# Kernel optimization log

Hardware: AMD Instinct MI355X
Metric: run time of the kernel (lower is better)

## Reference

```python
import jax, jax.numpy as jnp
import numpy as np

B, SQ, SK, H, NH = 2, 2048, 2048, 1024, 16
HD = H // NH  # 64


def setup_inputs() -> dict:
    key = jax.random.key(0)
    ks = jax.random.split(key, 12)
    s = 1.0 / np.sqrt(H)
    inp = {
        "query": jax.random.normal(ks[0], (B, SQ, H), jnp.float32),
        "key": jax.random.normal(ks[1], (B, SK, H), jnp.float32),
        "value": jax.random.normal(ks[2], (B, SK, H), jnp.float32),
        # lower-triangular causal mask [B, SQ, SK]; nonzero = attend
        "causal_mask": jnp.broadcast_to(
            jnp.tril(jnp.ones((SQ, SK), jnp.int32)), (B, SQ, SK)
        ),
        "Wq": jax.random.uniform(ks[3], (H, H), jnp.float32, -s, s),
        "bq": jnp.zeros((H,), jnp.float32),
        "Wk": jax.random.uniform(ks[4], (H, H), jnp.float32, -s, s),
        "bk": jnp.zeros((H,), jnp.float32),
        "Wv": jax.random.uniform(ks[5], (H, H), jnp.float32, -s, s),
        "bv": jnp.zeros((H,), jnp.float32),
        "Wo": jax.random.uniform(ks[6], (H, H), jnp.float32, -s, s),
        "bo": jnp.zeros((H,), jnp.float32),
        "ln_g": jnp.ones((H,), jnp.float32),
        "ln_b": jnp.zeros((H,), jnp.float32),
    }
    return inp


def _layer_norm(x, g, b, eps=1e-5):
    mu = jnp.mean(x, axis=-1, keepdims=True)
    var = jnp.var(x, axis=-1, keepdims=True)
    return (x - mu) * jax.lax.rsqrt(var + eps) * g + b


def reference(query, key, value, causal_mask, Wq, bq, Wk, bk, Wv, bv, Wo, bo, ln_g, ln_b):
    # projections (torch Linear: x @ W.T + b)
    q = (query @ Wq.T + bq).reshape(B, SQ, NH, HD)
    k = (key @ Wk.T + bk).reshape(B, SK, NH, HD)
    v = (value @ Wv.T + bv).reshape(B, SK, NH, HD)
    # scores [B, NH, SQ, SK]
    scores = jnp.einsum("bqhd,bkhd->bhqk", q, k) / np.sqrt(HD).astype(np.float32)
    scores = jnp.where(causal_mask[:, None, :, :] == 0, -jnp.inf, scores)
    attn = jax.nn.softmax(scores, axis=-1)
    # dropout is identity in eval mode
    out = jnp.einsum("bhqk,bkhd->bqhd", attn, v).reshape(B, SQ, H)
    out = out @ Wo.T + bo
    return _layer_norm(query + out, ln_g, ln_b)
```

## Files before the change

### kernel.cpp

```cpp
#include <hip/hip_runtime.h>
#include <hip/hip_bf16.h>

#define SQL 2048
#define SKL 2048
#define HH  1024
#define NHH 16
#define HDD 64
#define BB  2
#define MM  (BB*SQL)

typedef __attribute__((ext_vector_type(8))) short short8;
typedef __attribute__((ext_vector_type(4))) short short4v;
typedef __attribute__((ext_vector_type(4))) float f32x4;
typedef unsigned short u16;

__device__ inline u16 f2bf(float f) {
    unsigned int u = __float_as_uint(f);
    u += 0x7fffu + ((u >> 16) & 1u);
    return (u16)(u >> 16);
}

__device__ inline unsigned int bf2_bits(float a, float b) {
    __hip_bfloat162 h = __float22bfloat162_rn(make_float2(a, b));
    unsigned int r;
    __builtin_memcpy(&r, &h, 4);
    return r;
}

__device__ inline void gl_lds16(const void* g, void* l) {
    __builtin_amdgcn_global_load_lds(
        (const __attribute__((address_space(1))) unsigned int*)g,
        (__attribute__((address_space(3))) unsigned int*)l, 16, 0, 0);
}

__global__ __launch_bounds__(256) void cvt_all_kernel(
    const float* __restrict__ q, const float* __restrict__ k, const float* __restrict__ v,
    const float* __restrict__ wq, const float* __restrict__ wk,
    const float* __restrict__ wv, const float* __restrict__ wo,
    u16* __restrict__ xq, u16* __restrict__ xk, u16* __restrict__ xv,
    u16* __restrict__ wqb, u16* __restrict__ wkb, u16* __restrict__ wvb, u16* __restrict__ wob)
{
    int b = blockIdx.x;
    const float* src; u16* dst;
    if      (b < 4096)  { src = q;  dst = xq; }
    else if (b < 8192)  { src = k;  dst = xk;  b -= 4096; }
    else if (b < 12288) { src = v;  dst = xv;  b -= 8192; }
    else if (b < 13312) { src = wq; dst = wqb; b -= 12288; }
    else if (b < 14336) { src = wk; dst = wkb; b -= 13312; }
    else if (b < 15360) { src = wv; dst = wvb; b -= 14336; }
    else                { src = wo; dst = wob; b -= 15360; }
    int i = (b * 256 + threadIdx.x) * 4;
    float4 vv = *(const float4*)(src + i);
    ushort4 oo;
    oo.x = f2bf(vv.x); oo.y = f2bf(vv.y); oo.z = f2bf(vv.z); oo.w = f2bf(vv.w);
    *(ushort4*)(dst + i) = oo;
}

__global__ __launch_bounds__(256) void proj_kernel(
    const u16* __restrict__ xq, const u16* __restrict__ xk, const u16* __restrict__ xv,
    const u16* __restrict__ wqb, const u16* __restrict__ wkb, const u16* __restrict__ wvb,
    const float* __restrict__ bq, const float* __restrict__ bk, const float* __restrict__ bv,
    u16* __restrict__ oq, u16* __restrict__ ok, u16* __restrict__ ov)
{
    const int z = blockIdx.z;
    const u16* A      = (z == 0) ? xq  : (z == 1) ? xk  : xv;
    const u16* W      = (z == 0) ? wqb : (z == 1) ? wkb : wvb;
    const float* bias = (z == 0) ? bq  : (z == 1) ? bk  : bv;
    u16* outb         = (z == 0) ? oq  : (z == 1) ? ok  : ov;
    const float scale = (z == 0) ? 0.125f * 1.4426950408889634f : 1.0f;

    __shared__ u16 pool[2 * 128 * 64];
    u16* lds_a = pool;
    u16* lds_b = pool + 128 * 64;

    const int t = threadIdx.x;
    const int lane = t & 63;
    const int quad = lane >> 4;
    const int lo = lane & 15;
    const int wv = t >> 6;
    const int wm = (wv >> 1) * 64, wn = (wv & 1) * 64;
    const int m0 = blockIdx.x * 128;
    const int n0 = blockIdx.y * 128;

    f32x4 acc[4][4];
#pragma unroll
    for (int i = 0; i < 4; i++)
#pragma unroll
        for (int j = 0; j < 4; j++) acc[i][j] = (f32x4){0.f, 0.f, 0.f, 0.f};

    int rr[4], cc[4];
#pragma unroll
    for (int u = 0; u < 4; u++) {
        int sl = u * 256 + t;
        rr[u] = sl >> 3;
        cc[u] = ((sl & 7) ^ (rr[u] & 7)) * 8;
    }

    for (int k0 = 0; k0 < HH; k0 += 64) {
#pragma unroll
        for (int u = 0; u < 4; u++) {
            gl_lds16(A + (size_t)(m0 + rr[u]) * HH + k0 + cc[u], &lds_a[(u * 256 + t) * 8]);
            gl_lds16(W + (size_t)(n0 + rr[u]) * HH + k0 + cc[u], &lds_b[(u * 256 + t) * 8]);
        }
        __syncthreads();
#pragma unroll
        for (int kk = 0; kk < 2; kk++) {
            short8 af[4], bf[4];
#pragma unroll
            for (int i = 0; i < 4; i++) {
                const int ra = wm + i * 16 + lo;
                const int rb = wn + i * 16 + lo;
                af[i] = *(const short8*)&lds_a[ra * 64 + (((kk * 4 + quad) ^ (ra & 7)) * 8)];
                bf[i] = *(const short8*)&lds_b[rb * 64 + (((kk * 4 + quad) ^ (rb & 7)) * 8)];
            }
            if (z == 2) {
#pragma unroll
                for (int i = 0; i < 4; i++)
#pragma unroll
                    for (int j = 0; j < 4; j++)
                        acc[i][j] = __builtin_amdgcn_mfma_f32_16x16x32_bf16(af[i], bf[j], acc[i][j], 0, 0, 0);
            } else {
#pragma unroll
                for (int i = 0; i < 4; i++)
#pragma unroll
                    for (int j = 0; j < 4; j++)
                        acc[i][j] = __builtin_amdgcn_mfma_f32_16x16x32_bf16(bf[j], af[i], acc[i][j], 0, 0, 0);
            }
        }
        __syncthreads();
    }

    u16* cbuf = &pool[wv * 4096];

    if (z != 2) {
#pragma unroll
        for (int j = 0; j < 4; j++) {
            float4 b4 = *(const float4*)&bias[n0 + wn + j * 16 + quad * 4];
#pragma unroll
            for (int i = 0; i < 4; i++) {
                int tokl = i * 16 + lo;
                int lc = j * 2 + (quad >> 1);
                int phys = lc ^ (tokl & 7);
                uint2 pk;
                pk.x = bf2_bits((acc[i][j][0] + b4.x) * scale, (acc[i][j][1] + b4.y) * scale);
                pk.y = bf2_bits((acc[i][j][2] + b4.z) * scale, (acc[i][j][3] + b4.w) * scale);
                *(uint2*)&cbuf[tokl * 64 + phys * 8 + (quad & 1) * 4] = pk;
            }
        }
        __syncthreads();
#pragma unroll
        for (int it = 0; it < 8; it++) {
            int row = it * 8 + (lane >> 3);
            int lc2 = lane & 7;
            short8 val = *(const short8*)&cbuf[row * 64 + ((lc2 ^ (row & 7)) * 8)];
            int tok = m0 + wm + row;
            int dgb = n0 + wn + lc2 * 8;
            int bi = tok >> 11, s = tok & 2047;
            int head = dgb >> 6, d = dgb & 63;
            *(short8*)&outb[(((size_t)bi * NHH + head) * SQL + s) * HDD + d] = val;
        }
    } else {
#pragma unroll
        for (int j = 0; j < 4; j++) {
            float bsc = bias[n0 + wn + j * 16 + lo];
#pragma unroll
            for (int i = 0; i < 4; i++) {
                int dgl = j * 16 + lo;
                int lc = i * 2 + (quad >> 1);
                int phys = lc ^ (dgl & 7);
                uint2 pk;
                pk.x = bf2_bits(acc[i][j][0] + bsc, acc[i][j][1] + bsc);
                pk.y = bf2_bits(acc[i][j][2] + bsc, acc[i][j][3] + bsc);
                *(uint2*)&cbuf[dgl * 64 + phys * 8 + (quad & 1) * 4] = pk;
            }
        }
        __syncthreads();
#pragma unroll
        for (int it = 0; it < 8; it++) {
            int row = it * 8 + (lane >> 3);
            int lc2 = lane & 7;
            short8 val = *(const short8*)&cbuf[row * 64 + ((lc2 ^ (row & 7)) * 8)];
            int dg = n0 + wn + row;
            int tokb = m0 + wm + lc2 * 8;
            int bi = tokb >> 11, s = tokb & 2047;
            int head = dg >> 6, d = dg & 63;
            *(short8*)&outb[(((size_t)bi * NHH + head) * HDD + d) * SKL + s] = val;
        }
    }
}

__global__ __launch_bounds__(256) void outproj_kernel(
    const u16* __restrict__ A, const u16* __restrict__ W,
    const float* __restrict__ bias, const float* __restrict__ resid,
    float* __restrict__ outf)
{
    __shared__ u16 pool[2 * 128 * 64];
    u16* lds_a = pool;
    u16* lds_b = pool + 128 * 64;

    const int t = threadIdx.x;
    const int lane = t & 63;
    const int quad = lane >> 4;
    const int lo = lane & 15;
    const int wv = t >> 6;
    const int wm = (wv >> 1) * 64, wn = (wv & 1) * 64;
    const int m0 = blockIdx.x * 128;
    const int n0 = blockIdx.y * 128;

    f32x4 acc[4][4];
#pragma unroll
    for (int i = 0; i < 4; i++)
#pragma unroll
        for (int j = 0; j < 4; j++) acc[i][j] = (f32x4){0.f, 0.f, 0.f, 0.f};

    int rr[4], cc[4];
#pragma unroll
    for (int u = 0; u < 4; u++) {
        int sl = u * 256 + t;
        rr[u] = sl >> 3;
        cc[u] = ((sl & 7) ^ (rr[u] & 7)) * 8;
    }

    for (int k0 = 0; k0 < HH; k0 += 64) {
#pragma unroll
        for (int u = 0; u < 4; u++) {
            gl_lds16(A + (size_t)(m0 + rr[u]) * HH + k0 + cc[u], &lds_a[(u * 256 + t) * 8]);
            gl_lds16(W + (size_t)(n0 + rr[u]) * HH + k0 + cc[u], &lds_b[(u * 256 + t) * 8]);
        }
        __syncthreads();
#pragma unroll
        for (int kk = 0; kk < 2; kk++) {
            short8 af[4], bf[4];
#pragma unroll
            for (int i = 0; i < 4; i++) {
                const int ra = wm + i * 16 + lo;
                const int rb = wn + i * 16 + lo;
                af[i] = *(const short8*)&lds_a[ra * 64 + (((kk * 4 + quad) ^ (ra & 7)) * 8)];
                bf[i] = *(const short8*)&lds_b[rb * 64 + (((kk * 4 + quad) ^ (rb & 7)) * 8)];
            }
#pragma unroll
            for (int i = 0; i < 4; i++)
#pragma unroll
                for (int j = 0; j < 4; j++)
                    acc[i][j] = __builtin_amdgcn_mfma_f32_16x16x32_bf16(bf[j], af[i], acc[i][j], 0, 0, 0);
        }
        __syncthreads();
    }

    float* cbuf = (float*)&pool[wv * 4096];

#pragma unroll
    for (int half = 0; half < 2; half++) {
#pragma unroll
        for (int j = 0; j < 4; j++) {
            float4 b4 = *(const float4*)&bias[n0 + wn + j * 16 + quad * 4];
#pragma unroll
            for (int ii = 0; ii < 2; ii++) {
                int i = half * 2 + ii;
                int tl = ii * 16 + lo;
                int lc = j * 4 + quad;
                int phys = lc ^ (tl & 7);
                f32x4 vq;
                vq[0] = acc[i][j][0] + b4.x; vq[1] = acc[i][j][1] + b4.y;
                vq[2] = acc[i][j][2] + b4.z; vq[3] = acc[i][j][3] + b4.w;
                *(f32x4*)&cbuf[tl * 64 + phys * 4] = vq;
            }
        }
        __syncthreads();
#pragma unroll
        for (int it = 0; it < 8; it++) {
            int rowl = it * 4 + (lane >> 4);
            int lc2 = lane & 15;
            f32x4 val = *(const f32x4*)&cbuf[rowl * 64 + ((lc2 ^ (rowl & 7)) * 4)];
            int tok = m0 + wm + half * 32 + rowl;
            int col = n0 + wn + lc2 * 4;
            const float4 rd = *(const float4*)&resid[(size_t)tok * HH + col];
            float4 o;
            o.x = val[0] + rd.x; o.y = val[1] + rd.y;
            o.z = val[2] + rd.z; o.w = val[3] + rd.w;
            *(float4*)&outf[(size_t)tok * HH + col] = o;
        }
        __syncthreads();
    }
}

#define PSTR 72

__global__ __launch_bounds__(256) void attn_kernel(
    const u16* __restrict__ qb, const u16* __restrict__ kb, const u16* __restrict__ vtb,
    u16* __restrict__ attn_out)
{
    __shared__ u16 k_lds[64 * 64];
    __shared__ u16 vt_lds[64 * 64];
    __shared__ u16 p_lds[4 * 16 * PSTR];

    const int t = threadIdx.x;
    const int lane = t & 63;
    const int quad = lane >> 4;
    const int lo = lane & 15;
    const int w = t >> 6;
    const int qt = (SQL / 64 - 1) - (blockIdx.x >> 5);
    const int bh = blockIdx.x & 31;
    const int q0 = qt * 64;

    const u16* qbase = qb + ((size_t)bh * SQL + q0 + w * 16 + lo) * HDD + quad * 8;
    short8 qf0 = *(const short8*)qbase;
    short8 qf1 = *(const short8*)(qbase + 32);

    float m_s = -__builtin_inff(), l_s = 0.f;
    f32x4 o[4];
#pragma unroll
    for (int j = 0; j < 4; j++) o[j] = (f32x4){0.f, 0.f, 0.f, 0.f};

    const int sl0 = t, sl1 = 256 + t;
    const int r0 = sl0 >> 3, c0 = ((sl0 & 7) ^ (r0 & 7)) * 8;
    const int r1 = sl1 >> 3, c1 = ((sl1 & 7) ^ (r1 & 7)) * 8;
    const u16* kbh = kb + (size_t)bh * SKL * HDD;
    const u16* vbh = vtb + (size_t)bh * HDD * SKL;
    u16* ppriv = &p_lds[w * 16 * PSTR];

    for (int kt = 0; kt <= qt; kt++) {
        const int k0 = kt * 64;
        gl_lds16(kbh + (size_t)(k0 + r0) * HDD + c0, &k_lds[sl0 * 8]);
        gl_lds16(kbh + (size_t)(k0 + r1) * HDD + c1, &k_lds[sl1 * 8]);
        gl_lds16(vbh + (size_t)r0 * SKL + k0 + c0, &vt_lds[sl0 * 8]);
        gl_lds16(vbh + (size_t)r1 * SKL + k0 + c1, &vt_lds[sl1 * 8]);
        __syncthreads();

        f32x4 s[4];
#pragma unroll
        for (int nt = 0; nt < 4; nt++) {
            const int row = nt * 16 + lo;
            short8 kf0 = *(const short8*)&k_lds[row * 64 + ((quad ^ (row & 7)) * 8)];
            short8 kf1 = *(const short8*)&k_lds[row * 64 + (((4 + quad) ^ (row & 7)) * 8)];
            s[nt] = (f32x4){0.f, 0.f, 0.f, 0.f};
            s[nt] = __builtin_amdgcn_mfma_f32_16x16x32_bf16(kf0, qf0, s[nt], 0, 0, 0);
            s[nt] = __builtin_amdgcn_mfma_f32_16x16x32_bf16(kf1, qf1, s[nt], 0, 0, 0);
        }
        if (kt == qt) {
            const int ql = w * 16 + lo;
#pragma unroll
            for (int nt = 0; nt < 4; nt++)
#pragma unroll
                for (int r = 0; r < 4; r++)
                    if (nt * 16 + quad * 4 + r > ql) s[nt][r] = -__builtin_inff();
        }

        float mx = s[0][0];
#pragma unroll
        for (int nt = 0; nt < 4; nt++)
#pragma unroll
            for (int r = 0; r < 4; r++) mx = fmaxf(mx, s[nt][r]);
        mx = fmaxf(mx, __shfl_xor(mx, 16));
        mx = fmaxf(mx, __shfl_xor(mx, 32));
        float mnew = fmaxf(m_s, mx);
        float al = __builtin_amdgcn_exp2f(m_s - mnew);
        m_s = mnew;
        float rs = 0.f;
#pragma unroll
        for (int nt = 0; nt < 4; nt++)
#pragma unroll
            for (int r = 0; r < 4; r++) {
                s[nt][r] = __builtin_amdgcn_exp2f(s[nt][r] - m_s);
                rs += s[nt][r];
            }
        rs += __shfl_xor(rs, 16);
        rs += __shfl_xor(rs, 32);
        l_s = l_s * al + rs;

        float alr[4];
#pragma unroll
        for (int r = 0; r < 4; r++) alr[r] = __shfl(al, quad * 4 + r, 16);
#pragma unroll
        for (int nt = 0; nt < 4; nt++)
#pragma unroll
            for (int r = 0; r < 4; r++) o[nt][r] *= alr[r];

#pragma unroll
        for (int nt = 0; nt < 4; nt++) {
            short4v pk;
#pragma unroll
            for (int r = 0; r < 4; r++) pk[r] = (short)f2bf(s[nt][r]);
            *(short4v*)&ppriv[lo * PSTR + nt * 16 + quad * 4] = pk;
        }
        short8 pf0 = *(const short8*)&ppriv[lo * PSTR + quad * 8];
        short8 pf1 = *(const short8*)&ppriv[lo * PSTR + 32 + quad * 8];

#pragma unroll
        for (int nt = 0; nt < 4; nt++) {
            const int row = nt * 16 + lo;
            short8 vf0 = *(const short8*)&vt_lds[row * 64 + ((quad ^ (row & 7)) * 8)];
            short8 vf1 = *(const short8*)&vt_lds[row * 64 + (((4 + quad) ^ (row & 7)) * 8)];
            o[nt] = __builtin_amdgcn_mfma_f32_16x16x32_bf16(pf0, vf0, o[nt], 0, 0, 0);
            o[nt] = __builtin_amdgcn_mfma_f32_16x16x32_bf16(pf1, vf1, o[nt], 0, 0, 0);
        }
        __syncthreads();
    }

    const int b = bh >> 4, h = bh & 15;
    float inv[4];
#pragma unroll
    for (int r = 0; r < 4; r++) inv[r] = 1.0f / __shfl(l_s, quad * 4 + r, 16);
#pragma unroll
    for (int nt = 0; nt < 4; nt++)
#pragma unroll
        for (int r = 0; r < 4; r++) {
            int srow = q0 + w * 16 + quad * 4 + r;
            attn_out[((size_t)b * SQL + srow) * HH + h * HDD + nt * 16 + lo] =
                f2bf(o[nt][r] * inv[r]);
        }
}

__global__ __launch_bounds__(256) void ln_kernel(const float* __restrict__ x,
                                                 const float* __restrict__ g,
                                                 const float* __restrict__ bb,
                                                 float* __restrict__ out)
{
    const int row = blockIdx.x;
    const int t = threadIdx.x;
    const float* xr = x + (size_t)row * HH;
    float4 v = *(const float4*)(xr + t * 4);
    float s1 = v.x + v.y + v.z + v.w;
    float s2 = v.x * v.x + v.y * v.y + v.z * v.z + v.w * v.w;
#pragma unroll
    for (int off = 32; off; off >>= 1) { s1 += __shfl_xor(s1, off); s2 += __shfl_xor(s2, off); }
    __shared__ float red[8];
    if ((t & 63) == 0) { red[(t >> 6) * 2] = s1; red[(t >> 6) * 2 + 1] = s2; }
    __syncthreads();
    s1 = red[0] + red[2] + red[4] + red[6];
    s2 = red[1] + red[3] + red[5] + red[7];
    float mu = s1 * (1.0f / HH);
    float var = s2 * (1.0f / HH) - mu * mu;
    float rstd = rsqrtf(var + 1e-5f);
    float4 gg = *(const float4*)(g + t * 4);
    float4 b4 = *(const float4*)(bb + t * 4);
    float4 o;
    o.x = (v.x - mu) * rstd * gg.x + b4.x;
    o.y = (v.y - mu) * rstd * gg.y + b4.y;
    o.z = (v.z - mu) * rstd * gg.z + b4.z;
    o.w = (v.w - mu) * rstd * gg.w + b4.w;
    *(float4*)(out + (size_t)row * HH + t * 4) = o;
}

extern "C" void kernel_launch(void* const* d_in, const int* in_sizes, int n_in,
                              void* d_out, int out_size, void* d_ws, size_t ws_size,
                              hipStream_t stream)
{
    const float* query = (const float*)d_in[0];
    const float* key   = (const float*)d_in[1];
    const float* value = (const float*)d_in[2];
    const float* Wq = (const float*)d_in[4];
    const float* bq = (const float*)d_in[5];
    const float* Wk = (const float*)d_in[6];
    const float* bk = (const float*)d_in[7];
    const float* Wv = (const float*)d_in[8];
    const float* bv = (const float*)d_in[9];
    const float* Wo = (const float*)d_in[10];
    const float* bo = (const float*)d_in[11];
    const float* ln_g = (const float*)d_in[12];
    const float* ln_b = (const float*)d_in[13];
    float* out = (float*)d_out;

    char* wp = (char*)d_ws;
    auto alloc = [&](size_t bytes) { void* p = (void*)wp; wp += (bytes + 255) & ~(size_t)255; return p; };
    const int nW = HH * HH;
    const int nX = MM * HH;
    u16* wqb = (u16*)alloc((size_t)nW * 2);
    u16* wkb = (u16*)alloc((size_t)nW * 2);
    u16* wvb = (u16*)alloc((size_t)nW * 2);
    u16* wob = (u16*)alloc((size_t)nW * 2);
    u16* xq  = (u16*)alloc((size_t)nX * 2);
    u16* xk  = (u16*)alloc((size_t)nX * 2);
    u16* xv  = (u16*)alloc((size_t)nX * 2);
    u16* qbuf = (u16*)alloc((size_t)nX * 2);
    u16* kbuf = (u16*)alloc((size_t)nX * 2);
    u16* vbuf = (u16*)alloc((size_t)nX * 2);
    u16* attnb = (u16*)alloc((size_t)nX * 2);
    float* projf = (float*)alloc((size_t)nX * 4);

    cvt_all_kernel<<<16384, 256, 0, stream>>>(query, key, value, Wq, Wk, Wv, Wo,
                                              xq, xk, xv, wqb, wkb, wvb, wob);

    proj_kernel<<<dim3(32, 8, 3), 256, 0, stream>>>(
        xq, xk, xv, wqb, wkb, wvb, bq, bk, bv, qbuf, kbuf, vbuf);

    attn_kernel<<<1024, 256, 0, stream>>>(qbuf, kbuf, vbuf, attnb);

    outproj_kernel<<<dim3(32, 8), 256, 0, stream>>>(attnb, wob, bo, query, projf);

    ln_kernel<<<MM, 256, 0, stream>>>(projf, ln_g, ln_b, out);
}
```

Measured before the change: 253.9 us.

## Fuse fp32-to-bf16 activation conversion into projection GEMM and shrink outproj tiles

The separate conversion of query/key/value to bf16 is removed. The projection kernel now loads fp32 activations directly, converts them in registers and stores bf16 into LDS, which drops a full read-write pass over three 16MB inputs. The output projection tile shrinks from 128x128 to 64x128, doubling the grid to 512 blocks for better CU occupancy. In exchange, the projection kernel's A-operand loads are now synchronous register loads instead of async global-to-LDS, which may add latency in the GEMM loop.

```diff
diff --git a/kernel.cpp b/kernel.cpp
--- a/kernel.cpp
+++ b/kernel.cpp
@@ -33,22 +33,17 @@
         (__attribute__((address_space(3))) unsigned int*)l, 16, 0, 0);
 }
 
-__global__ __launch_bounds__(256) void cvt_all_kernel(
-    const float* __restrict__ q, const float* __restrict__ k, const float* __restrict__ v,
+__global__ __launch_bounds__(256) void cvt_w_kernel(
     const float* __restrict__ wq, const float* __restrict__ wk,
     const float* __restrict__ wv, const float* __restrict__ wo,
-    u16* __restrict__ xq, u16* __restrict__ xk, u16* __restrict__ xv,
     u16* __restrict__ wqb, u16* __restrict__ wkb, u16* __restrict__ wvb, u16* __restrict__ wob)
 {
     int b = blockIdx.x;
     const float* src; u16* dst;
-    if      (b < 4096)  { src = q;  dst = xq; }
-    else if (b < 8192)  { src = k;  dst = xk;  b -= 4096; }
-    else if (b < 12288) { src = v;  dst = xv;  b -= 8192; }
-    else if (b < 13312) { src = wq; dst = wqb; b -= 12288; }
-    else if (b < 14336) { src = wk; dst = wkb; b -= 13312; }
-    else if (b < 15360) { src = wv; dst = wvb; b -= 14336; }
-    else                { src = wo; dst = wob; b -= 15360; }
+    if      (b < 1024) { src = wq; dst = wqb; }
+    else if (b < 2048) { src = wk; dst = wkb; b -= 1024; }
+    else if (b < 3072) { src = wv; dst = wvb; b -= 2048; }
+    else               { src = wo; dst = wob; b -= 3072; }
     int i = (b * 256 + threadIdx.x) * 4;
     float4 vv = *(const float4*)(src + i);
     ushort4 oo;
@@ -57,13 +52,13 @@
 }
 
 __global__ __launch_bounds__(256) void proj_kernel(
-    const u16* __restrict__ xq, const u16* __restrict__ xk, const u16* __restrict__ xv,
+    const float* __restrict__ qf, const float* __restrict__ kf, const float* __restrict__ vf,
     const u16* __restrict__ wqb, const u16* __restrict__ wkb, const u16* __restrict__ wvb,
     const float* __restrict__ bq, const float* __restrict__ bk, const float* __restrict__ bv,
     u16* __restrict__ oq, u16* __restrict__ ok, u16* __restrict__ ov)
 {
     const int z = blockIdx.z;
-    const u16* A      = (z == 0) ? xq  : (z == 1) ? xk  : xv;
+    const float* A    = (z == 0) ? qf  : (z == 1) ? kf  : vf;
     const u16* W      = (z == 0) ? wqb : (z == 1) ? wkb : wvb;
     const float* bias = (z == 0) ? bq  : (z == 1) ? bk  : bv;
     u16* outb         = (z == 0) ? oq  : (z == 1) ? ok  : ov;
@@ -97,10 +92,22 @@
     }
 
     for (int k0 = 0; k0 < HH; k0 += 64) {
+        float4 a0[4], a1[4];
 #pragma unroll
         for (int u = 0; u < 4; u++) {
-            gl_lds16(A + (size_t)(m0 + rr[u]) * HH + k0 + cc[u], &lds_a[(u * 256 + t) * 8]);
+            const float* src = A + (size_t)(m0 + rr[u]) * HH + k0 + cc[u];
+            a0[u] = *(const float4*)src;
+            a1[u] = *(const float4*)(src + 4);
             gl_lds16(W + (size_t)(n0 + rr[u]) * HH + k0 + cc[u], &lds_b[(u * 256 + t) * 8]);
+        }
+#pragma unroll
+        for (int u = 0; u < 4; u++) {
+            uint4 pk;
+            pk.x = bf2_bits(a0[u].x, a0[u].y);
+            pk.y = bf2_bits(a0[u].z, a0[u].w);
+            pk.z = bf2_bits(a1[u].x, a1[u].y);
+            pk.w = bf2_bits(a1[u].z, a1[u].w);
+            *(uint4*)&lds_a[(u * 256 + t) * 8] = pk;
         }
         __syncthreads();
 #pragma unroll
@@ -196,20 +203,20 @@
 {
     __shared__ u16 pool[2 * 128 * 64];
     u16* lds_a = pool;
-    u16* lds_b = pool + 128 * 64;
+    u16* lds_b = pool + 64 * 64;
 
     const int t = threadIdx.x;
     const int lane = t & 63;
     const int quad = lane >> 4;
     const int lo = lane & 15;
     const int wv = t >> 6;
-    const int wm = (wv >> 1) * 64, wn = (wv & 1) * 64;
-    const int m0 = blockIdx.x * 128;
+    const int wm = (wv >> 1) * 32, wn = (wv & 1) * 64;
+    const int m0 = blockIdx.x * 64;
     const int n0 = blockIdx.y * 128;
 
-    f32x4 acc[4][4];
-#pragma unroll
-    for (int i = 0; i < 4; i++)
+    f32x4 acc[2][4];
+#pragma unroll
+    for (int i = 0; i < 2; i++)
 #pragma unroll
         for (int j = 0; j < 4; j++) acc[i][j] = (f32x4){0.f, 0.f, 0.f, 0.f};
 
@@ -223,23 +230,27 @@
 
     for (int k0 = 0; k0 < HH; k0 += 64) {
 #pragma unroll
-        for (int u = 0; u < 4; u++) {
+        for (int u = 0; u < 2; u++)
             gl_lds16(A + (size_t)(m0 + rr[u]) * HH + k0 + cc[u], &lds_a[(u * 256 + t) * 8]);
+#pragma unroll
+        for (int u = 0; u < 4; u++)
             gl_lds16(W + (size_t)(n0 + rr[u]) * HH + k0 + cc[u], &lds_b[(u * 256 + t) * 8]);
-        }
         __syncthreads();
 #pragma unroll
         for (int kk = 0; kk < 2; kk++) {
-            short8 af[4], bf[4];
-#pragma unroll
-            for (int i = 0; i < 4; i++) {
+            short8 af[2], bf[4];
+#pragma unroll
+            for (int i = 0; i < 2; i++) {
                 const int ra = wm + i * 16 + lo;
-                const int rb = wn + i * 16 + lo;
                 af[i] = *(const short8*)&lds_a[ra * 64 + (((kk * 4 + quad) ^ (ra & 7)) * 8)];
-                bf[i] = *(const short8*)&lds_b[rb * 64 + (((kk * 4 + quad) ^ (rb & 7)) * 8)];
-            }
-#pragma unroll
-            for (int i = 0; i < 4; i++)
+            }
+#pragma unroll
+            for (int j = 0; j < 4; j++) {
+                const int rb = wn + j * 16 + lo;
+                bf[j] = *(const short8*)&lds_b[rb * 64 + (((kk * 4 + quad) ^ (rb & 7)) * 8)];
+            }
+#pragma unroll
+            for (int i = 0; i < 2; i++)
 #pragma unroll
                 for (int j = 0; j < 4; j++)
                     acc[i][j] = __builtin_amdgcn_mfma_f32_16x16x32_bf16(bf[j], af[i], acc[i][j], 0, 0, 0);
@@ -248,39 +259,32 @@
     }
 
     float* cbuf = (float*)&pool[wv * 4096];
-
-#pragma unroll
-    for (int half = 0; half < 2; half++) {
-#pragma unroll
-        for (int j = 0; j < 4; j++) {
-            float4 b4 = *(const float4*)&bias[n0 + wn + j * 16 + quad * 4];
-#pragma unroll
-            for (int ii = 0; ii < 2; ii++) {
-                int i = half * 2 + ii;
-                int tl = ii * 16 + lo;
-                int lc = j * 4 + quad;
-                int phys = lc ^ (tl & 7);
-                f32x4 vq;
-                vq[0] = acc[i][j][0] + b4.x; vq[1] = acc[i][j][1] + b4.y;
-                vq[2] = acc[i][j][2] + b4.z; vq[3] = acc[i][j][3] + b4.w;
-                *(f32x4*)&cbuf[tl * 64 + phys * 4] = vq;
-            }
-        }
-        __syncthreads();
-#pragma unroll
-        for (int it = 0; it < 8; it++) {
-            int rowl = it * 4 + (lane >> 4);
-            int lc2 = lane & 15;
-            f32x4 val = *(const f32x4*)&cbuf[rowl * 64 + ((lc2 ^ (rowl & 7)) * 4)];
-            int tok = m0 + wm + half * 32 + rowl;
-            int col = n0 + wn + lc2 * 4;
-            const float4 rd = *(const float4*)&resid[(size_t)tok * HH + col];
-            float4 o;
-            o.x = val[0] + rd.x; o.y = val[1] + rd.y;
-            o.z = val[2] + rd.z; o.w = val[3] + rd.w;
-            *(float4*)&outf[(size_t)tok * HH + col] = o;
-        }
-        __syncthreads();
+#pragma unroll
+    for (int j = 0; j < 4; j++) {
+        float4 b4 = *(const float4*)&bias[n0 + wn + j * 16 + quad * 4];
+#pragma unroll
+        for (int i = 0; i < 2; i++) {
+            int tl = i * 16 + lo;
+            int lc = j * 4 + quad;
+            int phys = lc ^ (tl & 7);
+            f32x4 vq;
+            vq[0] = acc[i][j][0] + b4.x; vq[1] = acc[i][j][1] + b4.y;
+            vq[2] = acc[i][j][2] + b4.z; vq[3] = acc[i][j][3] + b4.w;
+            *(f32x4*)&cbuf[tl * 64 + phys * 4] = vq;
+        }
+    }
+#pragma unroll
+    for (int it = 0; it < 8; it++) {
+        int rowl = it * 4 + (lane >> 4);
+        int lc2 = lane & 15;
+        f32x4 val = *(const f32x4*)&cbuf[rowl * 64 + ((lc2 ^ (rowl & 7)) * 4)];
+        int tok = m0 + wm + rowl;
+        int col = n0 + wn + lc2 * 4;
+        const float4 rd = *(const float4*)&resid[(size_t)tok * HH + col];
+        float4 o;
+        o.x = val[0] + rd.x; o.y = val[1] + rd.y;
+        o.z = val[2] + rd.z; o.w = val[3] + rd.w;
+        *(float4*)&outf[(size_t)tok * HH + col] = o;
     }
 }
 
@@ -469,24 +473,20 @@
     u16* wkb = (u16*)alloc((size_t)nW * 2);
     u16* wvb = (u16*)alloc((size_t)nW * 2);
     u16* wob = (u16*)alloc((size_t)nW * 2);
-    u16* xq  = (u16*)alloc((size_t)nX * 2);
-    u16* xk  = (u16*)alloc((size_t)nX * 2);
-    u16* xv  = (u16*)alloc((size_t)nX * 2);
     u16* qbuf = (u16*)alloc((size_t)nX * 2);
     u16* kbuf = (u16*)alloc((size_t)nX * 2);
     u16* vbuf = (u16*)alloc((size_t)nX * 2);
     u16* attnb = (u16*)alloc((size_t)nX * 2);
     float* projf = (float*)alloc((size_t)nX * 4);
 
-    cvt_all_kernel<<<16384, 256, 0, stream>>>(query, key, value, Wq, Wk, Wv, Wo,
-                                              xq, xk, xv, wqb, wkb, wvb, wob);
+    cvt_w_kernel<<<4096, 256, 0, stream>>>(Wq, Wk, Wv, Wo, wqb, wkb, wvb, wob);
 
     proj_kernel<<<dim3(32, 8, 3), 256, 0, stream>>>(
-        xq, xk, xv, wqb, wkb, wvb, bq, bk, bv, qbuf, kbuf, vbuf);
+        query, key, value, wqb, wkb, wvb, bq, bk, bv, qbuf, kbuf, vbuf);
 
     attn_kernel<<<1024, 256, 0, stream>>>(qbuf, kbuf, vbuf, attnb);
 
-    outproj_kernel<<<dim3(32, 8), 256, 0, stream>>>(attnb, wob, bo, query, projf);
+    outproj_kernel<<<dim3(64, 8), 256, 0, stream>>>(attnb, wob, bo, query, projf);
 
     ln_kernel<<<MM, 256, 0, stream>>>(projf, ln_g, ln_b, out);
 }
```

After: 258.0 us. Within noise of the previous version (+1.6%).
